# Performance work log

Measured on AMD Instinct MI355X. Metric: run time of the kernel, lower is better.

The kernel has to match this reference:

```python
import math
import jax, jax.numpy as jnp
import numpy as np

C_CURV = 0.5  # Poincare ball curvature c (StablePoincareBall default)


def expmap0(u, c=C_CURV):
    """StablePoincareBall.expmap0: tangent at origin -> ball, with norm clamps."""
    sqrt_c = math.sqrt(c)
    u_norm = jnp.clip(jnp.linalg.norm(u, axis=-1, keepdims=True), 1e-8, 5.0)
    res = jnp.tanh(sqrt_c * u_norm) / sqrt_c * (u / u_norm)
    max_allowed = 0.95 / sqrt_c
    rn = jnp.linalg.norm(res, axis=-1, keepdims=True)
    scale = jnp.where(rn > max_allowed, max_allowed / rn, jnp.ones_like(rn))
    return res * scale


def poincare_pairwise_dist(x, p, c=C_CURV):
    """Geodesic dist d(x_i, p_j) = (2/sqrt(c)) atanh(sqrt(c) ||(-x) (+) p||).
    Uses the closed form for ||mobius_add(-x, p)||^2 in terms of ||x||^2, ||p||^2,
    <x,p> so only [B,C] intermediates are formed (no [B,C,D] broadcast).
    """
    x2 = jnp.sum(x * x, axis=-1, keepdims=True)        # [B,1]
    p2 = jnp.sum(p * p, axis=-1)[None, :]              # [1,C]
    mdot = -(x @ p.T)                                  # <-x, p>  [B,C]
    A = 1.0 + 2.0 * c * mdot + c * p2                  # coeff of (-x)
    Bc = 1.0 - c * x2                                  # coeff of p
    den = 1.0 + 2.0 * c * mdot + (c * c) * x2 * p2
    num2 = A * A * x2 + 2.0 * A * Bc * mdot + Bc * Bc * p2
    m2 = jnp.maximum(num2, 0.0) / jnp.maximum(den * den, 1e-15)
    sqrt_c = math.sqrt(c)
    arg = jnp.clip(sqrt_c * jnp.sqrt(m2 + 1e-15), 0.0, 1.0 - 1e-5)
    return (2.0 / sqrt_c) * jnp.arctanh(arg)


def setup_inputs() -> dict:
    key = jax.random.key(0)
    k1, k2 = jax.random.split(key)
    B, C, D = 128, 4096, 1024
    # inputs live on the Poincare ball: map random tangents via expmap0
    x = expmap0(0.5 * jax.random.normal(k1, (B, D), dtype=jnp.float32))
    # prototypes per __init__: expmap0(randn*0.1) then rescale norm to 1/sqrt(c)-1e-5
    init_tangent = 0.1 * jax.random.normal(k2, (C, D), dtype=jnp.float32)
    protos = expmap0(init_tangent)
    max_norm = 1.0 / math.sqrt(C_CURV) - 1e-5
    nrm = jnp.clip(jnp.linalg.norm(protos, axis=-1, keepdims=True), 1e-8)
    protos = protos * (max_norm / nrm)
    return {"x": x, "prototypes": protos}


def reference(x, prototypes):
    # logits = -geodesic distance to each class prototype, [B, num_classes]
    return -poincare_pairwise_dist(x, prototypes)
```

## Files before the change

kernel.cpp:

```cpp
#include <hip/hip_runtime.h>
#include <math.h>


#define DDIM 1024
#define CDIM 4096
#define RSTR 1040
#define PSOFF 33280

using f32x4 = __attribute__((ext_vector_type(4))) float;
using i32x4 = __attribute__((ext_vector_type(4))) int;

__global__ __launch_bounds__(256, 2) void hyper_fp8(
    const float* __restrict__ x, const float* __restrict__ p, float* __restrict__ out) {
  __shared__ __align__(16) char smem[66816];
  float* x2s = (float*)(smem + 66560);
  float* p2s = (float*)(smem + 66560 + 128);

  const int tid  = threadIdx.x;
  const int lane = tid & 63;
  const int w    = __builtin_amdgcn_readfirstlane(tid >> 6);
  const int r15  = lane & 15, g = lane >> 4;

  const int bid  = blockIdx.x;
  const int swz  = ((bid & 7) << 6) | (bid >> 3);
  const int rg   = swz & 3, cg = swz >> 2;
  const int rbase = rg * 32, cbase = cg * 32;

  const int srow = tid >> 3;
  const int l8   = tid & 7;
  const float* gx = x + (size_t)(rbase + srow) * DDIM + l8 * 16;
  const float* gp = p + (size_t)(cbase + srow) * DDIM + l8 * 16;
  char* xd = smem + srow * RSTR + l8 * 16;
  char* pd = smem + PSOFF + srow * RSTR + l8 * 16;

  float sx = 0.f, sp = 0.f;

  #pragma unroll
  for (int m = 0; m < 8; ++m) {
    f32x4 xv[4], pv[4];
    #pragma unroll
    for (int j = 0; j < 4; ++j) {
      xv[j] = *(const f32x4*)(gx + m * 128 + j * 4);
      pv[j] = *(const f32x4*)(gp + m * 128 + j * 4);
    }
    i32x4 xq, pq;
    #pragma unroll
    for (int j = 0; j < 4; ++j) {
      sx = fmaf(xv[j][0], xv[j][0], sx); sx = fmaf(xv[j][1], xv[j][1], sx);
      sx = fmaf(xv[j][2], xv[j][2], sx); sx = fmaf(xv[j][3], xv[j][3], sx);
      sp = fmaf(pv[j][0], pv[j][0], sp); sp = fmaf(pv[j][1], pv[j][1], sp);
      sp = fmaf(pv[j][2], pv[j][2], sp); sp = fmaf(pv[j][3], pv[j][3], sp);
      int xw = __builtin_amdgcn_cvt_pk_fp8_f32(xv[j][0], xv[j][1], 0, false);
      xw     = __builtin_amdgcn_cvt_pk_fp8_f32(xv[j][2], xv[j][3], xw, true);
      int pw = __builtin_amdgcn_cvt_pk_fp8_f32(pv[j][0], pv[j][1], 0, false);
      pw     = __builtin_amdgcn_cvt_pk_fp8_f32(pv[j][2], pv[j][3], pw, true);
      xq[j] = xw; pq[j] = pw;
    }
    *(i32x4*)(xd + m * 128) = xq;
    *(i32x4*)(pd + m * 128) = pq;
  }

  sx += __shfl_xor(sx, 1, 64); sx += __shfl_xor(sx, 2, 64); sx += __shfl_xor(sx, 4, 64);
  sp += __shfl_xor(sp, 1, 64); sp += __shfl_xor(sp, 2, 64); sp += __shfl_xor(sp, 4, 64);
  if ((lane & 7) == 0) { x2s[srow] = sx; p2s[srow] = sp; }

  __syncthreads();

  const int qr = w & 1, qc = w >> 1;
  const char* abase = smem + (qr * 16 + r15) * RSTR + g * 8;
  const char* bbase = smem + PSOFF + (qc * 16 + r15) * RSTR + g * 8;
  f32x4 acc = {0.f, 0.f, 0.f, 0.f};
  #pragma unroll
  for (int kk = 0; kk < 32; ++kk) {
    const long a = *(const long*)(abase + kk * 32);
    const long b = *(const long*)(bbase + kk * 32);
    acc = __builtin_amdgcn_mfma_f32_16x16x32_fp8_fp8(a, b, acc, 0, 0, 0);
  }

  const float p2 = p2s[qc * 16 + r15];
  #pragma unroll
  for (int i = 0; i < 4; ++i) {
    const int  rloc = qr * 16 + (g << 2) + i;
    const float dot = acc[i];
    const float x2  = x2s[rloc];
    const float A   = 1.0f - dot + 0.5f  * p2;
    const float Bc  = 1.0f - 0.5f * x2;
    const float den = 1.0f - dot + 0.25f * x2 * p2;
    float num2 = A * A * x2 - 2.0f * A * Bc * dot + Bc * Bc * p2;
    float m2   = fmaxf(num2, 0.0f) / fmaxf(den * den, 1e-15f);
    float arg  = fminf(0.7071067811865476f * sqrtf(m2 + 1e-15f), 0.99999f);
    out[(size_t)(rbase + rloc) * CDIM + cbase + qc * 16 + r15] =
        -1.4142135623730951f * __logf((1.0f + arg) / (1.0f - arg));
  }
}

extern "C" void kernel_launch(void* const* d_in, const int* in_sizes, int n_in,
                              void* d_out, int out_size, void* d_ws, size_t ws_size,
                              hipStream_t stream) {
  const float* x = (const float*)d_in[0];
  const float* p = (const float*)d_in[1];
  float* out = (float*)d_out;
  hyper_fp8<<<dim3(512), dim3(256), 0, stream>>>(x, p, out);
}
```

Measured before the change: 16.01 us.

## Stream prototypes from global into registers with bf16 MFMA and 32x64 tiles

Restructures the kernel so only the x tile (32 rows, bf16, XOR-swizzled) is staged in shared memory. Each wave streams its 16 prototype rows straight from global memory into registers with a 4-deep prefetch, converting to bf16 and accumulating p-norms on the fly. Tiles grow to 32x64 with 256 blocks, halving x re-staging and removing the p shared-memory round trip. The cost is bf16 in place of fp8 MFMA (more bytes and MFMA work, better precision), fewer blocks, and per-lane strided global loads for p.

```diff
diff --git a/kernel.cpp b/kernel.cpp
--- a/kernel.cpp
+++ b/kernel.cpp
@@ -1,20 +1,24 @@
 #include <hip/hip_runtime.h>
+#include <hip/hip_bf16.h>
 #include <math.h>
 
 
 #define DDIM 1024
 #define CDIM 4096
-#define RSTR 1040
-#define PSOFF 33280
 
-using f32x4 = __attribute__((ext_vector_type(4))) float;
-using i32x4 = __attribute__((ext_vector_type(4))) int;
+using f32x4  = __attribute__((ext_vector_type(4))) float;
+using bf16x8 = __attribute__((ext_vector_type(8))) short;
 
-__global__ __launch_bounds__(256, 2) void hyper_fp8(
-    const float* __restrict__ x, const float* __restrict__ p, float* __restrict__ out) {
-  __shared__ __align__(16) char smem[66816];
-  float* x2s = (float*)(smem + 66560);
-  float* p2s = (float*)(smem + 66560 + 128);
+__device__ inline ushort toBfU(float f) {
+  __hip_bfloat16 h = __float2bfloat16(f);
+  return *reinterpret_cast<ushort*>(&h);
+}
+
+__global__ __launch_bounds__(256) void hyper_pstream(
+    const float* __restrict__ x, const float* __restrict__ p,
+    float* __restrict__ out) {
+  __shared__ __align__(16) char xs[32 * 2048];
+  __shared__ float x2s[32];
 
   const int tid  = threadIdx.x;
   const int lane = tid & 63;
@@ -22,75 +26,106 @@
   const int r15  = lane & 15, g = lane >> 4;
 
   const int bid  = blockIdx.x;
-  const int swz  = ((bid & 7) << 6) | (bid >> 3);
-  const int rg   = swz & 3, cg = swz >> 2;
-  const int rbase = rg * 32, cbase = cg * 32;
+  const int swz  = ((bid & 7) << 5) | (bid >> 3);
+  const int cg   = swz >> 2, rg = swz & 3;
+  const int rbase = rg * 32, cbase = cg * 64;
 
-  const int srow = tid >> 3;
-  const int l8   = tid & 7;
-  const float* gx = x + (size_t)(rbase + srow) * DDIM + l8 * 16;
-  const float* gp = p + (size_t)(cbase + srow) * DDIM + l8 * 16;
-  char* xd = smem + srow * RSTR + l8 * 16;
-  char* pd = smem + PSOFF + srow * RSTR + l8 * 16;
+  const int tr = tid >> 3, l8 = tid & 7;
+  const float* gx = x + (size_t)(rbase + tr) * DDIM + l8 * 16;
+  const int xsw = (tr & 7) << 4;
 
-  float sx = 0.f, sp = 0.f;
-
+  float sx = 0.f;
   #pragma unroll
   for (int m = 0; m < 8; ++m) {
-    f32x4 xv[4], pv[4];
-    #pragma unroll
-    for (int j = 0; j < 4; ++j) {
-      xv[j] = *(const f32x4*)(gx + m * 128 + j * 4);
-      pv[j] = *(const f32x4*)(gp + m * 128 + j * 4);
-    }
-    i32x4 xq, pq;
-    #pragma unroll
-    for (int j = 0; j < 4; ++j) {
-      sx = fmaf(xv[j][0], xv[j][0], sx); sx = fmaf(xv[j][1], xv[j][1], sx);
-      sx = fmaf(xv[j][2], xv[j][2], sx); sx = fmaf(xv[j][3], xv[j][3], sx);
-      sp = fmaf(pv[j][0], pv[j][0], sp); sp = fmaf(pv[j][1], pv[j][1], sp);
-      sp = fmaf(pv[j][2], pv[j][2], sp); sp = fmaf(pv[j][3], pv[j][3], sp);
-      int xw = __builtin_amdgcn_cvt_pk_fp8_f32(xv[j][0], xv[j][1], 0, false);
-      xw     = __builtin_amdgcn_cvt_pk_fp8_f32(xv[j][2], xv[j][3], xw, true);
-      int pw = __builtin_amdgcn_cvt_pk_fp8_f32(pv[j][0], pv[j][1], 0, false);
-      pw     = __builtin_amdgcn_cvt_pk_fp8_f32(pv[j][2], pv[j][3], pw, true);
-      xq[j] = xw; pq[j] = pw;
-    }
-    *(i32x4*)(xd + m * 128) = xq;
-    *(i32x4*)(pd + m * 128) = pq;
+    f32x4 v0 = *(const f32x4*)(gx + m * 128);
+    f32x4 v1 = *(const f32x4*)(gx + m * 128 + 4);
+    f32x4 v2 = *(const f32x4*)(gx + m * 128 + 8);
+    f32x4 v3 = *(const f32x4*)(gx + m * 128 + 12);
+    sx = fmaf(v0[0],v0[0],sx); sx = fmaf(v0[1],v0[1],sx);
+    sx = fmaf(v0[2],v0[2],sx); sx = fmaf(v0[3],v0[3],sx);
+    sx = fmaf(v1[0],v1[0],sx); sx = fmaf(v1[1],v1[1],sx);
+    sx = fmaf(v1[2],v1[2],sx); sx = fmaf(v1[3],v1[3],sx);
+    sx = fmaf(v2[0],v2[0],sx); sx = fmaf(v2[1],v2[1],sx);
+    sx = fmaf(v2[2],v2[2],sx); sx = fmaf(v2[3],v2[3],sx);
+    sx = fmaf(v3[0],v3[0],sx); sx = fmaf(v3[1],v3[1],sx);
+    sx = fmaf(v3[2],v3[2],sx); sx = fmaf(v3[3],v3[3],sx);
+    bf16x8 wlo, whi;
+    wlo[0]=(short)toBfU(v0[0]); wlo[1]=(short)toBfU(v0[1]);
+    wlo[2]=(short)toBfU(v0[2]); wlo[3]=(short)toBfU(v0[3]);
+    wlo[4]=(short)toBfU(v1[0]); wlo[5]=(short)toBfU(v1[1]);
+    wlo[6]=(short)toBfU(v1[2]); wlo[7]=(short)toBfU(v1[3]);
+    whi[0]=(short)toBfU(v2[0]); whi[1]=(short)toBfU(v2[1]);
+    whi[2]=(short)toBfU(v2[2]); whi[3]=(short)toBfU(v2[3]);
+    whi[4]=(short)toBfU(v3[0]); whi[5]=(short)toBfU(v3[1]);
+    whi[6]=(short)toBfU(v3[2]); whi[7]=(short)toBfU(v3[3]);
+    const int kb = m * 256 + l8 * 32;
+    *(bf16x8*)&xs[tr * 2048 + ((kb)      ^ xsw)] = wlo;
+    *(bf16x8*)&xs[tr * 2048 + ((kb + 16) ^ xsw)] = whi;
   }
+  sx += __shfl_xor(sx, 1, 64);
+  sx += __shfl_xor(sx, 2, 64);
+  sx += __shfl_xor(sx, 4, 64);
+  if ((lane & 7) == 0) x2s[tr] = sx;
 
-  sx += __shfl_xor(sx, 1, 64); sx += __shfl_xor(sx, 2, 64); sx += __shfl_xor(sx, 4, 64);
-  sp += __shfl_xor(sp, 1, 64); sp += __shfl_xor(sp, 2, 64); sp += __shfl_xor(sp, 4, 64);
-  if ((lane & 7) == 0) { x2s[srow] = sx; p2s[srow] = sp; }
+  const float* gp = p + (size_t)(cbase + w * 16 + r15) * DDIM + g * 8;
+  f32x4 pb[4][2];
+  #pragma unroll
+  for (int kk = 0; kk < 4; ++kk) {
+    pb[kk][0] = *(const f32x4*)(gp + kk * 32);
+    pb[kk][1] = *(const f32x4*)(gp + kk * 32 + 4);
+  }
 
   __syncthreads();
 
-  const int qr = w & 1, qc = w >> 1;
-  const char* abase = smem + (qr * 16 + r15) * RSTR + g * 8;
-  const char* bbase = smem + PSOFF + (qc * 16 + r15) * RSTR + g * 8;
-  f32x4 acc = {0.f, 0.f, 0.f, 0.f};
+  const int a0base = r15 * 2048;
+  const int a1base = (16 + r15) * 2048;
+  const int aswz0  = (r15 & 7) << 4;
+  f32x4 acc0 = {0.f,0.f,0.f,0.f}, acc1 = {0.f,0.f,0.f,0.f};
+  float p2p = 0.f;
+
   #pragma unroll
   for (int kk = 0; kk < 32; ++kk) {
-    const long a = *(const long*)(abase + kk * 32);
-    const long b = *(const long*)(bbase + kk * 32);
-    acc = __builtin_amdgcn_mfma_f32_16x16x32_fp8_fp8(a, b, acc, 0, 0, 0);
+    const f32x4 q0 = pb[kk & 3][0], q1 = pb[kk & 3][1];
+    p2p = fmaf(q0[0],q0[0],p2p); p2p = fmaf(q0[1],q0[1],p2p);
+    p2p = fmaf(q0[2],q0[2],p2p); p2p = fmaf(q0[3],q0[3],p2p);
+    p2p = fmaf(q1[0],q1[0],p2p); p2p = fmaf(q1[1],q1[1],p2p);
+    p2p = fmaf(q1[2],q1[2],p2p); p2p = fmaf(q1[3],q1[3],p2p);
+    bf16x8 bb;
+    bb[0]=(short)toBfU(q0[0]); bb[1]=(short)toBfU(q0[1]);
+    bb[2]=(short)toBfU(q0[2]); bb[3]=(short)toBfU(q0[3]);
+    bb[4]=(short)toBfU(q1[0]); bb[5]=(short)toBfU(q1[1]);
+    bb[6]=(short)toBfU(q1[2]); bb[7]=(short)toBfU(q1[3]);
+    if (kk < 28) {
+      pb[kk & 3][0] = *(const f32x4*)(gp + (kk + 4) * 32);
+      pb[kk & 3][1] = *(const f32x4*)(gp + (kk + 4) * 32 + 4);
+    }
+    const int ko = kk * 64 + g * 16;
+    const bf16x8 a0 = *(const bf16x8*)&xs[a0base + (ko ^ aswz0)];
+    const bf16x8 a1 = *(const bf16x8*)&xs[a1base + (ko ^ aswz0)];
+    acc0 = __builtin_amdgcn_mfma_f32_16x16x32_bf16(a0, bb, acc0, 0, 0, 0);
+    acc1 = __builtin_amdgcn_mfma_f32_16x16x32_bf16(a1, bb, acc1, 0, 0, 0);
   }
 
-  const float p2 = p2s[qc * 16 + r15];
+  p2p += __shfl_xor(p2p, 16, 64);
+  p2p += __shfl_xor(p2p, 32, 64);
+  const float p2 = p2p;
+
   #pragma unroll
   for (int i = 0; i < 4; ++i) {
-    const int  rloc = qr * 16 + (g << 2) + i;
-    const float dot = acc[i];
-    const float x2  = x2s[rloc];
-    const float A   = 1.0f - dot + 0.5f  * p2;
-    const float Bc  = 1.0f - 0.5f * x2;
-    const float den = 1.0f - dot + 0.25f * x2 * p2;
-    float num2 = A * A * x2 - 2.0f * A * Bc * dot + Bc * Bc * p2;
-    float m2   = fmaxf(num2, 0.0f) / fmaxf(den * den, 1e-15f);
-    float arg  = fminf(0.7071067811865476f * sqrtf(m2 + 1e-15f), 0.99999f);
-    out[(size_t)(rbase + rloc) * CDIM + cbase + qc * 16 + r15] =
-        -1.4142135623730951f * __logf((1.0f + arg) / (1.0f - arg));
+    #pragma unroll
+    for (int f = 0; f < 2; ++f) {
+      const int  rloc = f * 16 + (g << 2) + i;
+      const float dot = f ? acc1[i] : acc0[i];
+      const float x2  = x2s[rloc];
+      const float A   = 1.0f - dot + 0.5f  * p2;
+      const float Bc  = 1.0f - 0.5f * x2;
+      const float den = 1.0f - dot + 0.25f * x2 * p2;
+      float num2 = A * A * x2 - 2.0f * A * Bc * dot + Bc * Bc * p2;
+      float m2   = fmaxf(num2, 0.0f) / fmaxf(den * den, 1e-15f);
+      float arg  = fminf(0.7071067811865476f * sqrtf(m2 + 1e-15f), 0.99999f);
+      out[(size_t)(rbase + rloc) * CDIM + cbase + w * 16 + r15] =
+          -1.4142135623730951f * __logf((1.0f + arg) / (1.0f - arg));
+    }
   }
 }
 
@@ -100,5 +135,5 @@
   const float* x = (const float*)d_in[0];
   const float* p = (const float*)d_in[1];
   float* out = (float*)d_out;
-  hyper_fp8<<<dim3(512), dim3(256), 0, stream>>>(x, p, out);
+  hyper_pstream<<<dim3(256), dim3(256), 0, stream>>>(x, p, out);
 }
```

Measured after the change: 17.44 us. 1.09x slower.
